# Optimization experiments

Hardware: AMD Instinct MI355X
Metric: run time of the kernel (lower is better)

## Reference

```python
import math
import jax, jax.numpy as jnp
import numpy as np

L, H, C, T_MAX, V = 4, 12, 768, 1024, 50257
D = C // H
EPS = 1e-5


def setup_inputs() -> dict:
    key = jax.random.key(0)
    ks = iter(jax.random.split(key, 32))
    s = 0.02
    inp = {
        "idx": jax.random.randint(next(ks), (2, 1024), 0, V, dtype=jnp.int32),
        "wte": jax.random.normal(next(ks), (V, C), jnp.float32) * s,
        "wpe": jax.random.normal(next(ks), (T_MAX, C), jnp.float32) * s,
        # per-layer stacked params, weights stored [in, out]
        "ln1_w": jnp.ones((L, C), jnp.float32),
        "ln1_b": jnp.zeros((L, C), jnp.float32),
        "qkv_w": jax.random.normal(next(ks), (L, C, 3 * C), jnp.float32) * s,
        "qkv_b": jnp.zeros((L, 3 * C), jnp.float32),
        "proj_w": jax.random.normal(next(ks), (L, C, C), jnp.float32) * (s / math.sqrt(2 * L)),
        "proj_b": jnp.zeros((L, C), jnp.float32),
        "ln2_w": jnp.ones((L, C), jnp.float32),
        "ln2_b": jnp.zeros((L, C), jnp.float32),
        "fc_w": jax.random.normal(next(ks), (L, C, 4 * C), jnp.float32) * s,
        "fc_b": jnp.zeros((L, 4 * C), jnp.float32),
        "fc2_w": jax.random.normal(next(ks), (L, 4 * C, C), jnp.float32) * (s / math.sqrt(2 * L)),
        "fc2_b": jnp.zeros((L, C), jnp.float32),
        "lnf_w": jnp.ones((C,), jnp.float32),
        "lnf_b": jnp.zeros((C,), jnp.float32),
        "head_w": jax.random.normal(next(ks), (C, V), jnp.float32) * s,
    }
    return inp


def _layernorm(x, w, b):
    mu = jnp.mean(x, axis=-1, keepdims=True)
    var = jnp.mean(jnp.square(x - mu), axis=-1, keepdims=True)
    return (x - mu) * jax.lax.rsqrt(var + EPS) * w + b


def _new_gelu(x):
    k = math.sqrt(2.0 / math.pi)
    return 0.5 * x * (1.0 + jnp.tanh(k * (x + 0.044715 * x * x * x)))


def _gpt_forward(idx, wte, wpe, layer_params, lnf_w, lnf_b, head_w):
    B, T = idx.shape
    x = wte[idx] + wpe[:T][None, :, :]  # [B, T, C]
    causal = jnp.tril(jnp.ones((T, T), bool))

    def block(x, p):
        ln1w, ln1b, qkvw, qkvb, pw, pb, ln2w, ln2b, fcw, fcb, fc2w, fc2b = p
        h = _layernorm(x, ln1w, ln1b)
        qkv = h @ qkvw + qkvb  # [B, T, 3C]
        q, k, v = jnp.split(qkv, 3, axis=-1)
        # [B, H, T, D]
        q = q.reshape(B, T, H, D).transpose(0, 2, 1, 3)
        k = k.reshape(B, T, H, D).transpose(0, 2, 1, 3)
        v = v.reshape(B, T, H, D).transpose(0, 2, 1, 3)
        att = jnp.einsum("bhtd,bhsd->bhts", q, k) * (1.0 / math.sqrt(D))
        att = jnp.where(causal, att, -jnp.inf)
        att = jax.nn.softmax(att, axis=-1)
        y = jnp.einsum("bhts,bhsd->bhtd", att, v)
        y = y.transpose(0, 2, 1, 3).reshape(B, T, C)
        x = x + (y @ pw + pb)
        h2 = _layernorm(x, ln2w, ln2b)
        m = _new_gelu(h2 @ fcw + fcb) @ fc2w + fc2b
        return x + m, None

    x, _ = jax.lax.scan(block, x, layer_params)
    x = _layernorm(x, lnf_w, lnf_b)
    logits = x @ head_w  # [B, T, V]
    return logits.reshape(B * T, V)


def reference(idx, wte, wpe, ln1_w, ln1_b, qkv_w, qkv_b, proj_w, proj_b,
              ln2_w, ln2_b, fc_w, fc_b, fc2_w, fc2_b, lnf_w, lnf_b, head_w):
    layer_params = (ln1_w, ln1_b, qkv_w, qkv_b, proj_w, proj_b,
                    ln2_w, ln2_b, fc_w, fc_b, fc2_w, fc2_b)
    return _gpt_forward(idx, wte, wpe, layer_params, lnf_w, lnf_b, head_w)
```

## Files before the change

kernel.cpp:

```cpp
#include <hip/hip_runtime.h>
#include <hip/hip_bf16.h>

typedef __hip_bfloat16 bf16;
typedef __attribute__((ext_vector_type(8))) short bf16x8;
typedef __attribute__((ext_vector_type(4))) float f32x4;
typedef __attribute__((ext_vector_type(4), aligned(4))) float f32x4u;

#define NL 4
#define NH 12
#define C 768
#define T 1024
#define NB 2
#define BTOK 2048
#define V 50257
#define DH 64

__device__ __forceinline__ void gload16(const void* g, void* l) {
  __builtin_amdgcn_global_load_lds(
      (const __attribute__((address_space(1))) void*)g,
      (__attribute__((address_space(3))) void*)l, 16, 0, 0);
}

__device__ __forceinline__ float block_sum(float v, float* red) {
#pragma unroll
  for (int off = 32; off; off >>= 1) v += __shfl_down(v, off);
  int lane = threadIdx.x & 63, wid = threadIdx.x >> 6;
  __syncthreads();
  if (lane == 0) red[wid] = v;
  __syncthreads();
  return red[0] + red[1] + red[2] + red[3];
}

__global__ __launch_bounds__(256) void k_transpose_bf16(const float* __restrict__ W,
    bf16* __restrict__ Wt, int K, int N) {
  __shared__ float tile[64][69];
  long zoff = (long)blockIdx.z * K * N;
  W += zoff;
  Wt += zoff;
  int k0 = blockIdx.x * 64, n0 = blockIdx.y * 64;
  int tid = threadIdx.x;
  int rr = tid >> 4, rc = (tid & 15) * 4;
#pragma unroll
  for (int it = 0; it < 4; it++) {
    int k = it * 16 + rr;
    int gn = n0 + rc;
    const float* src = W + (long)(k0 + k) * N + gn;
    if (gn + 3 < N) {
      f32x4 v = *(const f32x4u*)src;
      tile[k][rc] = v[0]; tile[k][rc + 1] = v[1];
      tile[k][rc + 2] = v[2]; tile[k][rc + 3] = v[3];
    } else {
#pragma unroll
      for (int e = 0; e < 4; e++)
        tile[k][rc + e] = (gn + e < N) ? src[e] : 0.0f;
    }
  }
  __syncthreads();
  int wkc = tid & 7;
#pragma unroll
  for (int it = 0; it < 2; it++) {
    int n = it * 32 + (tid >> 3);
    int gn = n0 + n;
    if (gn < N) {
      union { bf16 h[8]; bf16x8 v; } u;
#pragma unroll
      for (int j = 0; j < 8; j++)
        u.h[j] = __float2bfloat16(tile[wkc * 8 + j][n]);
      *(bf16x8*)&Wt[(long)gn * K + k0 + wkc * 8] = u.v;
    }
  }
}

__global__ __launch_bounds__(256) void k_layernorm(const float* __restrict__ x,
    const float* __restrict__ w, const float* __restrict__ b, bf16* __restrict__ out) {
  __shared__ float red[4];
  long row = blockIdx.x;
  const float* xr = x + row * C;
  int t = threadIdx.x;
  float v0 = xr[t], v1 = xr[t + 256], v2 = xr[t + 512];
  float s = block_sum(v0 + v1 + v2, red);
  float mu = s * (1.0f / C);
  float d0 = v0 - mu, d1 = v1 - mu, d2 = v2 - mu;
  float vs = block_sum(d0 * d0 + d1 * d1 + d2 * d2, red);
  float inv = rsqrtf(vs * (1.0f / C) + 1e-5f);
  bf16* orow = out + row * C;
  orow[t]       = __float2bfloat16(d0 * inv * w[t]       + b[t]);
  orow[t + 256] = __float2bfloat16(d1 * inv * w[t + 256] + b[t + 256]);
  orow[t + 512] = __float2bfloat16(d2 * inv * w[t + 512] + b[t + 512]);
}

__global__ __launch_bounds__(256) void k_embed_ln(const int* __restrict__ idx,
    const float* __restrict__ wte, const float* __restrict__ wpe,
    const float* __restrict__ w, const float* __restrict__ b,
    float* __restrict__ x, bf16* __restrict__ out) {
  __shared__ float red[4];
  long row = blockIdx.x;
  int t = threadIdx.x;
  int tok = idx[row];
  int pos = (int)(row & (T - 1));
  const float* we = wte + (long)tok * C;
  const float* pe = wpe + (long)pos * C;
  float v0 = we[t] + pe[t], v1 = we[t + 256] + pe[t + 256], v2 = we[t + 512] + pe[t + 512];
  float* xr = x + row * C;
  xr[t] = v0; xr[t + 256] = v1; xr[t + 512] = v2;
  float s = block_sum(v0 + v1 + v2, red);
  float mu = s * (1.0f / C);
  float d0 = v0 - mu, d1 = v1 - mu, d2 = v2 - mu;
  float vs = block_sum(d0 * d0 + d1 * d1 + d2 * d2, red);
  float inv = rsqrtf(vs * (1.0f / C) + 1e-5f);
  bf16* orow = out + row * C;
  orow[t]       = __float2bfloat16(d0 * inv * w[t]       + b[t]);
  orow[t + 256] = __float2bfloat16(d1 * inv * w[t + 256] + b[t + 256]);
  orow[t + 512] = __float2bfloat16(d2 * inv * w[t + 512] + b[t + 512]);
}

__global__ __launch_bounds__(256) void k_attn(const bf16* __restrict__ q,
    const bf16* __restrict__ k, const bf16* __restrict__ vt,
    bf16* __restrict__ yb) {
  __shared__ __align__(16) bf16 Pl[4][16][72];
  int pr = blockIdx.x, bh = blockIdx.y;
  int b = bh / NH, h = bh % NH;
  int tid = threadIdx.x, w = tid >> 6, lane = tid & 63;
  int l15 = lane & 15, hi = lane >> 4;
  const bf16* qbase = q + (long)bh * T * DH;
  const bf16* kbase = k + (long)bh * T * DH;
  const bf16* vbase = vt + (long)bh * DH * T;

  int qt = blockIdx.z ? (T / 64 - 1 - pr) : pr;
  int qrow = qt * 64 + w * 16 + l15;
  bf16x8 qf0 = *(const bf16x8*)(qbase + (long)qrow * DH + hi * 8);
  bf16x8 qf1 = *(const bf16x8*)(qbase + (long)qrow * DH + 32 + hi * 8);

  f32x4 accy[4] = {};
  float m_run = -1e30f, l_run = 0.f;

  int nkt = qt + 1;
  for (int kt = 0; kt < nkt; kt++) {
    int kv0 = kt * 64;
    f32x4 accs[4] = {};
#pragma unroll
    for (int kvi = 0; kvi < 4; kvi++) {
      const bf16* kr = kbase + (long)(kv0 + kvi * 16 + l15) * DH + hi * 8;
      bf16x8 kf0 = *(const bf16x8*)kr;
      bf16x8 kf1 = *(const bf16x8*)(kr + 32);
      accs[kvi] = __builtin_amdgcn_mfma_f32_16x16x32_bf16(kf0, qf0, accs[kvi], 0, 0, 0);
      accs[kvi] = __builtin_amdgcn_mfma_f32_16x16x32_bf16(kf1, qf1, accs[kvi], 0, 0, 0);
    }
    bool diag = (kt == qt);
    float p[4][4];
    float tmax = -1e30f;
#pragma unroll
    for (int kvi = 0; kvi < 4; kvi++)
#pragma unroll
      for (int rr = 0; rr < 4; rr++) {
        float s = accs[kvi][rr];
        if (diag && (kvi * 16 + hi * 4 + rr > w * 16 + l15)) s = -1e30f;
        p[kvi][rr] = s;
        tmax = fmaxf(tmax, s);
      }
    tmax = fmaxf(tmax, __shfl_xor(tmax, 16));
    tmax = fmaxf(tmax, __shfl_xor(tmax, 32));
    if (!__all(tmax - m_run <= 8.0f)) {
      float m_new = fmaxf(m_run, tmax);
      float scl = __expf(m_run - m_new);
      l_run *= scl;
#pragma unroll
      for (int rr = 0; rr < 4; rr++) {
        float sy = __shfl(scl, hi * 4 + rr);
#pragma unroll
        for (int j = 0; j < 4; j++) accy[j][rr] *= sy;
      }
      m_run = m_new;
    }
    float psum = 0.f;
#pragma unroll
    for (int kvi = 0; kvi < 4; kvi++)
#pragma unroll
      for (int rr = 0; rr < 4; rr++) {
        float e = __expf(p[kvi][rr] - m_run);
        p[kvi][rr] = e;
        psum += e;
      }
    psum += __shfl_xor(psum, 16);
    psum += __shfl_xor(psum, 32);
    l_run += psum;
#pragma unroll
    for (int kvi = 0; kvi < 4; kvi++) {
      union { bf16 hh[2]; unsigned u; } pk0, pk1;
      pk0.hh[0] = __float2bfloat16(p[kvi][0]);
      pk0.hh[1] = __float2bfloat16(p[kvi][1]);
      pk1.hh[0] = __float2bfloat16(p[kvi][2]);
      pk1.hh[1] = __float2bfloat16(p[kvi][3]);
      *(unsigned*)&Pl[w][l15][kvi * 16 + hi * 4]     = pk0.u;
      *(unsigned*)&Pl[w][l15][kvi * 16 + hi * 4 + 2] = pk1.u;
    }
#pragma unroll
    for (int c = 0; c < 2; c++) {
      bf16x8 pf = *(const bf16x8*)&Pl[w][l15][c * 32 + hi * 8];
#pragma unroll
      for (int j = 0; j < 4; j++) {
        const bf16* vr = vbase + (long)(j * 16 + l15) * T + kv0 + c * 32 + hi * 8;
        bf16x8 vf = *(const bf16x8*)vr;
        accy[j] = __builtin_amdgcn_mfma_f32_16x16x32_bf16(pf, vf, accy[j], 0, 0, 0);
      }
    }
  }
  float inv = 1.0f / l_run;
#pragma unroll
  for (int rr = 0; rr < 4; rr++) {
    float li = __shfl(inv, hi * 4 + rr);
    int qg = qt * 64 + w * 16 + hi * 4 + rr;
#pragma unroll
    for (int j = 0; j < 4; j++)
      yb[((long)(b * T + qg)) * C + h * DH + j * 16 + l15] =
          __float2bfloat16(accy[j][rr] * li);
  }
}

__global__ __launch_bounds__(512, 1) void k_head(const bf16* __restrict__ A,
    const bf16* __restrict__ B, float* __restrict__ Cv) {
  __shared__ __align__(16) char lds[131072];
  int hw = blockIdx.y * 8 + blockIdx.x;
  int L = (hw & 7) * 197 + (hw >> 3);
  int mt = L & 7, nt = L >> 3;
  int m0 = mt * 256, n0 = nt * 256;
  int tid = threadIdx.x, lane = tid & 63, wid = tid >> 6;
  int wm = wid >> 2, wn = wid & 3;
  int l15 = lane & 15, hi = lane >> 4, l7 = lane & 7;
  int sg = (lane & 7) ^ (lane >> 3);
  int srA = wid * 8 + (lane >> 3);
  const bf16* Ab = A + (long)(m0 + srA) * 768 + sg * 8;
  const bf16* Bb = B + (long)(n0 + srA) * 768 + sg * 8;
  auto STAGE = [&](int tile, int h) {
    char* dst = lds + (tile & 1) * 65536 + h * 16384 + wid * 1024;
    const bf16* src = (h < 2 ? Ab : Bb) + (long)((h & 1) * 128) * 768 + tile * 64;
    gload16(src, dst);
    gload16(src + 64 * 768, dst + 8192);
  };
  f32x4 acc[8][4] = {};
  STAGE(0, 0); STAGE(0, 1); STAGE(0, 2); STAGE(0, 3); STAGE(1, 0);
  asm volatile("s_waitcnt vmcnt(2)" ::: "memory");
  __builtin_amdgcn_s_barrier();
  int bro = (wn & 1) * 64;
  int g0 = (hi ^ l7) * 16, g1 = ((4 + hi) ^ l7) * 16;
  for (int t = 0; t < 12; t++) {
    char* ha = lds + (t & 1) * 65536 + wm * 16384;
    char* hb = lds + (t & 1) * 65536 + 32768 + (wn >> 1) * 16384;
    bf16x8 af[4], bv[4];
#pragma unroll
    for (int mf = 0; mf < 4; mf++)
      af[mf] = *(const bf16x8*)(ha + (mf * 16 + l15) * 128 + g0);
#pragma unroll
    for (int nf = 0; nf < 4; nf++)
      bv[nf] = *(const bf16x8*)(hb + (bro + nf * 16 + l15) * 128 + g0);
    if (t + 1 < 12) { STAGE(t + 1, 1); STAGE(t + 1, 2); }
    __builtin_amdgcn_s_barrier();
    __builtin_amdgcn_s_setprio(1);
#pragma unroll
    for (int mf = 0; mf < 4; mf++)
#pragma unroll
      for (int nf = 0; nf < 4; nf++)
        acc[mf][nf] = __builtin_amdgcn_mfma_f32_16x16x32_bf16(af[mf], bv[nf], acc[mf][nf], 0, 0, 0);
    __builtin_amdgcn_s_setprio(0);
    __builtin_amdgcn_s_barrier();
#pragma unroll
    for (int mf = 0; mf < 4; mf++)
      af[mf] = *(const bf16x8*)(ha + ((mf + 4) * 16 + l15) * 128 + g0);
    if (t + 1 < 12) STAGE(t + 1, 3);
    __builtin_amdgcn_s_barrier();
    __builtin_amdgcn_s_setprio(1);
#pragma unroll
    for (int mf = 0; mf < 4; mf++)
#pragma unroll
      for (int nf = 0; nf < 4; nf++)
        acc[mf + 4][nf] = __builtin_amdgcn_mfma_f32_16x16x32_bf16(af[mf], bv[nf], acc[mf + 4][nf], 0, 0, 0);
    __builtin_amdgcn_s_setprio(0);
    __builtin_amdgcn_s_barrier();
#pragma unroll
    for (int mf = 0; mf < 4; mf++)
      af[mf] = *(const bf16x8*)(ha + (mf * 16 + l15) * 128 + g1);
#pragma unroll
    for (int nf = 0; nf < 4; nf++)
      bv[nf] = *(const bf16x8*)(hb + (bro + nf * 16 + l15) * 128 + g1);
    __builtin_amdgcn_s_barrier();
    __builtin_amdgcn_s_setprio(1);
#pragma unroll
    for (int mf = 0; mf < 4; mf++)
#pragma unroll
      for (int nf = 0; nf < 4; nf++)
        acc[mf][nf] = __builtin_amdgcn_mfma_f32_16x16x32_bf16(af[mf], bv[nf], acc[mf][nf], 0, 0, 0);
    __builtin_amdgcn_s_setprio(0);
    __builtin_amdgcn_s_barrier();
#pragma unroll
    for (int mf = 0; mf < 4; mf++)
      af[mf] = *(const bf16x8*)(ha + ((mf + 4) * 16 + l15) * 128 + g1);
    if (t + 2 < 12) STAGE(t + 2, 0);
    __builtin_amdgcn_s_barrier();
    __builtin_amdgcn_s_setprio(1);
#pragma unroll
    for (int mf = 0; mf < 4; mf++)
#pragma unroll
      for (int nf = 0; nf < 4; nf++)
        acc[mf + 4][nf] = __builtin_amdgcn_mfma_f32_16x16x32_bf16(af[mf], bv[nf], acc[mf + 4][nf], 0, 0, 0);
    __builtin_amdgcn_s_setprio(0);
    if (t < 11) {
      if (t + 2 < 12) asm volatile("s_waitcnt vmcnt(2)" ::: "memory");
      else            asm volatile("s_waitcnt vmcnt(0)" ::: "memory");
      __builtin_amdgcn_s_barrier();
    }
  }
  __syncthreads();
  float* Cst = (float*)lds;
#pragma unroll
  for (int rnd = 0; rnd < 4; rnd++) {
#pragma unroll
    for (int mfl = 0; mfl < 2; mfl++) {
      int mf = rnd * 2 + mfl;
#pragma unroll
      for (int nf = 0; nf < 4; nf++)
#pragma unroll
        for (int rr = 0; rr < 4; rr++)
          Cst[(wm * 32 + mfl * 16 + hi * 4 + rr) * 260 + wn * 64 + nf * 16 + l15] =
              acc[mf][nf][rr];
    }
    __syncthreads();
#pragma unroll
    for (int s = 0; s < 8; s++) {
      int gid = tid + s * 512;
      int r = gid >> 6, g = gid & 63;
      int grow = m0 + (r >> 5) * 128 + (rnd * 2 + ((r >> 4) & 1)) * 16 + (r & 15);
      int gcol = n0 + g * 4;
      f32x4 vv = *(const f32x4*)&Cst[r * 260 + g * 4];
      float* dst = Cv + (long)grow * V + gcol;
      if (gcol + 3 < V) {
        *(f32x4u*)dst = vv;
      } else {
#pragma unroll
        for (int e = 0; e < 4; e++)
          if (gcol + e < V) dst[e] = vv[e];
      }
    }
    __syncthreads();
  }
}

#define SBK 64
template <int EPI>
__global__ __launch_bounds__(256) void k_gemm_s(const bf16* __restrict__ A,
    const bf16* __restrict__ B, const float* __restrict__ bias,
    void* __restrict__ Cv, int M, int N, int K, int lda, int ldb, int ldc,
    void* __restrict__ Cv2, void* __restrict__ Cv3) {
  __shared__ __align__(16) bf16 As[2][64][SBK];
  __shared__ __align__(16) bf16 Bs[2][128][SBK];
  int nwg = gridDim.x * gridDim.y;
  int hw = blockIdx.y * gridDim.x + blockIdx.x;
  int logical = (hw & 7) * (nwg >> 3) + (hw >> 3);
  int bx = logical % gridDim.x, by = logical / gridDim.x;
  int m0 = bx * 64, n0 = by * 128;
  int tid = threadIdx.x;
  int lane = tid & 63, w = tid >> 6;
  int l15 = lane & 15, hi = lane >> 4, l7 = lane & 7;
  int srow = lane >> 3;
  int sgr = lane & 7;
  int scol = ((sgr ^ srow) << 3);
  f32x4 acc[4][2] = {};
  const bf16* Ag = A + (long)(m0 + w * 8 + srow) * lda + scol;
  const bf16* Bg = B + (long)(n0 + w * 8 + srow) * ldb + scol;
  int NT = K / SBK;
  auto STAGE = [&](int t) {
    int k0 = t * SBK, b = t & 1;
    gload16(Ag + k0,            &As[b][w * 8][0]);
    gload16(Ag + k0 + 32 * lda, &As[b][w * 8 + 32][0]);
    gload16(Bg + k0,            &Bs[b][w * 8][0]);
    gload16(Bg + k0 + 32 * ldb, &Bs[b][w * 8 + 32][0]);
    gload16(Bg + k0 + 64 * ldb, &Bs[b][w * 8 + 64][0]);
    gload16(Bg + k0 + 96 * ldb, &Bs[b][w * 8 + 96][0]);
  };
  STAGE(0);
  STAGE(1);
  int c0 = (hi ^ l7) << 3, c1 = ((4 + hi) ^ l7) << 3;
  for (int t = 0; t < NT; t++) {
    int b = t & 1;
    if (t + 1 < NT) asm volatile("s_waitcnt vmcnt(6)" ::: "memory");
    else            asm volatile("s_waitcnt vmcnt(0)" ::: "memory");
    __builtin_amdgcn_s_barrier();
    bf16x8 a0[4], a1[4], b0[2], b1[2];
#pragma unroll
    for (int i = 0; i < 4; i++) {
      a0[i] = *(const bf16x8*)&As[b][i * 16 + l15][c0];
      a1[i] = *(const bf16x8*)&As[b][i * 16 + l15][c1];
    }
#pragma unroll
    for (int j = 0; j < 2; j++) {
      b0[j] = *(const bf16x8*)&Bs[b][w * 32 + j * 16 + l15][c0];
      b1[j] = *(const bf16x8*)&Bs[b][w * 32 + j * 16 + l15][c1];
    }
    asm volatile("s_waitcnt lgkmcnt(0)" ::: "memory");
    __builtin_amdgcn_s_barrier();
    if (t + 2 < NT) STAGE(t + 2);
    __builtin_amdgcn_s_setprio(1);
#pragma unroll
    for (int i = 0; i < 4; i++)
#pragma unroll
      for (int j = 0; j < 2; j++) {
        acc[i][j] = __builtin_amdgcn_mfma_f32_16x16x32_bf16(a0[i], b0[j], acc[i][j], 0, 0, 0);
        acc[i][j] = __builtin_amdgcn_mfma_f32_16x16x32_bf16(a1[i], b1[j], acc[i][j], 0, 0, 0);
      }
    __builtin_amdgcn_s_setprio(0);
  }
#pragma unroll
  for (int j = 0; j < 2; j++) {
    int gn = n0 + w * 32 + j * 16 + l15;
    float bv = bias[gn];
#pragma unroll
    for (int i = 0; i < 4; i++)
#pragma unroll
      for (int rr = 0; rr < 4; rr++) {
        int gm = m0 + i * 16 + hi * 4 + rr;
        float v = acc[i][j][rr] + bv;
        if constexpr (EPI == 3) {
          long off = (long)gm * ldc + gn;
          ((float*)Cv)[off] = v + ((float*)Cv)[off];
        } else if constexpr (EPI == 2) {
          float u = 0.7978845608028654f * (v + 0.044715f * v * v * v);
          u = fminf(fmaxf(u, -15.f), 15.f);
          float e2 = __expf(2.f * u);
          float th = (e2 - 1.f) / (e2 + 1.f);
          ((bf16*)Cv)[(long)gm * ldc + gn] = __float2bfloat16(0.5f * v * (1.f + th));
        } else if constexpr (EPI == 5) {
          int gb = gm >> 10, gt = gm & 1023;
          int which = gn / C;
          int r = gn - which * C;
          int h = r >> 6, d = r & 63;
          long bh = (long)(gb * NH + h);
          if (which == 0)
            ((bf16*)Cv)[(bh * T + gt) * DH + d] = __float2bfloat16(v * 0.125f);
          else if (which == 1)
            ((bf16*)Cv2)[(bh * T + gt) * DH + d] = __float2bfloat16(v);
          else
            ((bf16*)Cv3)[(bh * DH + d) * T + gt] = __float2bfloat16(v);
        }
      }
  }
}

extern "C" void kernel_launch(void* const* d_in, const int* in_sizes, int n_in,
                              void* d_out, int out_size, void* d_ws, size_t ws_size,
                              hipStream_t stream) {
  const int*   idx    = (const int*)d_in[0];
  const float* wte    = (const float*)d_in[1];
  const float* wpe    = (const float*)d_in[2];
  const float* ln1_w  = (const float*)d_in[3];
  const float* ln1_b  = (const float*)d_in[4];
  const float* qkv_w  = (const float*)d_in[5];
  const float* qkv_b  = (const float*)d_in[6];
  const float* proj_w = (const float*)d_in[7];
  const float* proj_b = (const float*)d_in[8];
  const float* ln2_w  = (const float*)d_in[9];
  const float* ln2_b  = (const float*)d_in[10];
  const float* fc_w   = (const float*)d_in[11];
  const float* fc_b   = (const float*)d_in[12];
  const float* fc2_w  = (const float*)d_in[13];
  const float* fc2_b  = (const float*)d_in[14];
  const float* lnf_w  = (const float*)d_in[15];
  const float* lnf_b  = (const float*)d_in[16];
  const float* head_w = (const float*)d_in[17];
  (void)in_sizes; (void)n_in; (void)out_size; (void)ws_size;

  char* base = (char*)d_ws;
  size_t off = 0;
  auto alloc = [&](size_t bytes) -> void* {
    void* p = base + off;
    off = (off + bytes + 255) & ~(size_t)255;
    return p;
  };
  bf16* wt_qkv  = (bf16*)alloc((size_t)NL * 3 * C * C * 2);
  bf16* wt_proj = (bf16*)alloc((size_t)NL * C * C * 2);
  bf16* wt_fc   = (bf16*)alloc((size_t)NL * 4 * C * C * 2);
  bf16* wt_fc2  = (bf16*)alloc((size_t)NL * 4 * C * C * 2);
  bf16* wt_head = (bf16*)alloc((size_t)V * C * 2);
  float* x      = (float*)alloc((size_t)BTOK * C * 4);
  bf16*  xb     = (bf16*)alloc((size_t)BTOK * C * 2);
  bf16*  qb     = (bf16*)alloc((size_t)NB * NH * T * DH * 2);
  bf16*  kb     = (bf16*)alloc((size_t)NB * NH * T * DH * 2);
  bf16*  vtb    = (bf16*)alloc((size_t)NB * NH * T * DH * 2);
  bf16*  yb     = (bf16*)alloc((size_t)BTOK * C * 2);
  bf16*  mbuf   = (bf16*)alloc((size_t)BTOK * 4 * C * 2);

  k_transpose_bf16<<<dim3(12, 36, NL), 256, 0, stream>>>(qkv_w, wt_qkv, C, 3 * C);
  k_transpose_bf16<<<dim3(12, 12, NL), 256, 0, stream>>>(proj_w, wt_proj, C, C);
  k_transpose_bf16<<<dim3(12, 48, NL), 256, 0, stream>>>(fc_w, wt_fc, C, 4 * C);
  k_transpose_bf16<<<dim3(48, 12, NL), 256, 0, stream>>>(fc2_w, wt_fc2, 4 * C, C);
  k_transpose_bf16<<<dim3(12, (V + 63) / 64, 1), 256, 0, stream>>>(head_w, wt_head, C, V);

  k_embed_ln<<<BTOK, 256, 0, stream>>>(idx, wte, wpe, ln1_w, ln1_b, x, xb);

  for (int l = 0; l < NL; l++) {
    if (l > 0)
      k_layernorm<<<BTOK, 256, 0, stream>>>(x, ln1_w + l * C, ln1_b + l * C, xb);
    k_gemm_s<5><<<dim3(32, 18), 256, 0, stream>>>(xb, wt_qkv + (long)l * 3 * C * C,
        qkv_b + l * 3 * C, qb, BTOK, 3 * C, C, C, C, 0, kb, vtb);
    k_attn<<<dim3(T / 128, NB * NH, 2), 256, 0, stream>>>(qb, kb, vtb, yb);
    k_gemm_s<3><<<dim3(32, 6), 256, 0, stream>>>(yb, wt_proj + (long)l * C * C,
        proj_b + l * C, x, BTOK, C, C, C, C, C, nullptr, nullptr);
    k_layernorm<<<BTOK, 256, 0, stream>>>(x, ln2_w + l * C, ln2_b + l * C, xb);
    k_gemm_s<2><<<dim3(32, 24), 256, 0, stream>>>(xb, wt_fc + (long)l * 4 * C * C,
        fc_b + l * 4 * C, mbuf, BTOK, 4 * C, C, C, C, 4 * C, nullptr, nullptr);
    k_gemm_s<3><<<dim3(32, 6), 256, 0, stream>>>(mbuf, wt_fc2 + (long)l * 4 * C * C,
        fc2_b + l * C, x, BTOK, C, 4 * C, 4 * C, 4 * C, C, nullptr, nullptr);
  }
  k_layernorm<<<BTOK, 256, 0, stream>>>(x, lnf_w, lnf_b, xb);
  k_head<<<dim3(8, 197), 512, 0, stream>>>(xb, wt_head, (float*)d_out);
}
```

Before: 986.0 us.

## Restructure LM-head GEMM with smaller K tiles and halved LDS for occupancy

Rewrites the vocab-projection GEMM main loop to use 32-wide K tiles (24 iterations) in a simple double-buffered LDS scheme with a new XOR swizzle, halving shared memory from 128KB to 64KB. It also raises the launch-bounds occupancy hint so more blocks can be resident per CU, and splits the epilogue into eight 16-row rounds. The aim is to hide latency through occupancy instead of the previous finely interleaved single-block schedule. The risk is register pressure: 128 accumulator floats under a higher occupancy hint may spill, and shorter K tiles mean more barriers per FLOP.

```diff
diff --git a/kernel.cpp b/kernel.cpp
--- a/kernel.cpp
+++ b/kernel.cpp
@@ -217,118 +217,74 @@
   }
 }
 
-__global__ __launch_bounds__(512, 1) void k_head(const bf16* __restrict__ A,
+__global__ __launch_bounds__(512, 4) void k_head(const bf16* __restrict__ A,
     const bf16* __restrict__ B, float* __restrict__ Cv) {
-  __shared__ __align__(16) char lds[131072];
+  __shared__ __align__(16) char lds[65536];
   int hw = blockIdx.y * 8 + blockIdx.x;
   int L = (hw & 7) * 197 + (hw >> 3);
   int mt = L & 7, nt = L >> 3;
   int m0 = mt * 256, n0 = nt * 256;
   int tid = threadIdx.x, lane = tid & 63, wid = tid >> 6;
   int wm = wid >> 2, wn = wid & 3;
-  int l15 = lane & 15, hi = lane >> 4, l7 = lane & 7;
-  int sg = (lane & 7) ^ (lane >> 3);
-  int srA = wid * 8 + (lane >> 3);
-  const bf16* Ab = A + (long)(m0 + srA) * 768 + sg * 8;
-  const bf16* Bb = B + (long)(n0 + srA) * 768 + sg * 8;
-  auto STAGE = [&](int tile, int h) {
-    char* dst = lds + (tile & 1) * 65536 + h * 16384 + wid * 1024;
-    const bf16* src = (h < 2 ? Ab : Bb) + (long)((h & 1) * 128) * 768 + tile * 64;
-    gload16(src, dst);
-    gload16(src + 64 * 768, dst + 8192);
+  int l15 = lane & 15, hi = lane >> 4;
+  int srow = lane >> 2;
+  int sgsrc = ((lane & 3) ^ ((lane >> 3) & 3)) * 8;
+  const bf16* Ag = A + (long)(m0 + srow) * 768 + sgsrc;
+  const bf16* Bg = B + (long)(n0 + srow) * 768 + sgsrc;
+  const int NT = 24;
+  auto STAGE = [&](int t) {
+    int k0 = t * 32, b = t & 1;
+#pragma unroll
+    for (int q = 0; q < 2; q++) {
+      int R0 = wid * 32 + q * 16;
+      gload16(Ag + (long)R0 * 768 + k0, lds + b * 16384 + R0 * 64);
+      gload16(Bg + (long)R0 * 768 + k0, lds + 32768 + b * 16384 + R0 * 64);
+    }
   };
   f32x4 acc[8][4] = {};
-  STAGE(0, 0); STAGE(0, 1); STAGE(0, 2); STAGE(0, 3); STAGE(1, 0);
-  asm volatile("s_waitcnt vmcnt(2)" ::: "memory");
-  __builtin_amdgcn_s_barrier();
-  int bro = (wn & 1) * 64;
-  int g0 = (hi ^ l7) * 16, g1 = ((4 + hi) ^ l7) * 16;
-  for (int t = 0; t < 12; t++) {
-    char* ha = lds + (t & 1) * 65536 + wm * 16384;
-    char* hb = lds + (t & 1) * 65536 + 32768 + (wn >> 1) * 16384;
-    bf16x8 af[4], bv[4];
-#pragma unroll
-    for (int mf = 0; mf < 4; mf++)
-      af[mf] = *(const bf16x8*)(ha + (mf * 16 + l15) * 128 + g0);
+  STAGE(0);
+  STAGE(1);
+  int gsw = (hi ^ ((l15 >> 1) & 3)) << 4;
+  for (int t = 0; t < NT; t++) {
+    int b = t & 1;
+    if (t + 1 < NT) asm volatile("s_waitcnt vmcnt(4)" ::: "memory");
+    else            asm volatile("s_waitcnt vmcnt(0)" ::: "memory");
+    __builtin_amdgcn_s_barrier();
+    bf16x8 af[8], bv[4];
+    char* ha = lds + b * 16384;
+    char* hb = lds + 32768 + b * 16384;
+#pragma unroll
+    for (int mf = 0; mf < 8; mf++)
+      af[mf] = *(const bf16x8*)(ha + (wm * 128 + mf * 16 + l15) * 64 + gsw);
 #pragma unroll
     for (int nf = 0; nf < 4; nf++)
-      bv[nf] = *(const bf16x8*)(hb + (bro + nf * 16 + l15) * 128 + g0);
-    if (t + 1 < 12) { STAGE(t + 1, 1); STAGE(t + 1, 2); }
+      bv[nf] = *(const bf16x8*)(hb + (wn * 64 + nf * 16 + l15) * 64 + gsw);
+    asm volatile("s_waitcnt lgkmcnt(0)" ::: "memory");
     __builtin_amdgcn_s_barrier();
+    if (t + 2 < NT) STAGE(t + 2);
     __builtin_amdgcn_s_setprio(1);
 #pragma unroll
-    for (int mf = 0; mf < 4; mf++)
+    for (int mf = 0; mf < 8; mf++)
 #pragma unroll
       for (int nf = 0; nf < 4; nf++)
         acc[mf][nf] = __builtin_amdgcn_mfma_f32_16x16x32_bf16(af[mf], bv[nf], acc[mf][nf], 0, 0, 0);
     __builtin_amdgcn_s_setprio(0);
-    __builtin_amdgcn_s_barrier();
-#pragma unroll
-    for (int mf = 0; mf < 4; mf++)
-      af[mf] = *(const bf16x8*)(ha + ((mf + 4) * 16 + l15) * 128 + g0);
-    if (t + 1 < 12) STAGE(t + 1, 3);
-    __builtin_amdgcn_s_barrier();
-    __builtin_amdgcn_s_setprio(1);
-#pragma unroll
-    for (int mf = 0; mf < 4; mf++)
-#pragma unroll
-      for (int nf = 0; nf < 4; nf++)
-        acc[mf + 4][nf] = __builtin_amdgcn_mfma_f32_16x16x32_bf16(af[mf], bv[nf], acc[mf + 4][nf], 0, 0, 0);
-    __builtin_amdgcn_s_setprio(0);
-    __builtin_amdgcn_s_barrier();
-#pragma unroll
-    for (int mf = 0; mf < 4; mf++)
-      af[mf] = *(const bf16x8*)(ha + (mf * 16 + l15) * 128 + g1);
-#pragma unroll
-    for (int nf = 0; nf < 4; nf++)
-      bv[nf] = *(const bf16x8*)(hb + (bro + nf * 16 + l15) * 128 + g1);
-    __builtin_amdgcn_s_barrier();
-    __builtin_amdgcn_s_setprio(1);
-#pragma unroll
-    for (int mf = 0; mf < 4; mf++)
-#pragma unroll
-      for (int nf = 0; nf < 4; nf++)
-        acc[mf][nf] = __builtin_amdgcn_mfma_f32_16x16x32_bf16(af[mf], bv[nf], acc[mf][nf], 0, 0, 0);
-    __builtin_amdgcn_s_setprio(0);
-    __builtin_amdgcn_s_barrier();
-#pragma unroll
-    for (int mf = 0; mf < 4; mf++)
-      af[mf] = *(const bf16x8*)(ha + ((mf + 4) * 16 + l15) * 128 + g1);
-    if (t + 2 < 12) STAGE(t + 2, 0);
-    __builtin_amdgcn_s_barrier();
-    __builtin_amdgcn_s_setprio(1);
-#pragma unroll
-    for (int mf = 0; mf < 4; mf++)
-#pragma unroll
-      for (int nf = 0; nf < 4; nf++)
-        acc[mf + 4][nf] = __builtin_amdgcn_mfma_f32_16x16x32_bf16(af[mf], bv[nf], acc[mf + 4][nf], 0, 0, 0);
-    __builtin_amdgcn_s_setprio(0);
-    if (t < 11) {
-      if (t + 2 < 12) asm volatile("s_waitcnt vmcnt(2)" ::: "memory");
-      else            asm volatile("s_waitcnt vmcnt(0)" ::: "memory");
-      __builtin_amdgcn_s_barrier();
-    }
   }
   __syncthreads();
   float* Cst = (float*)lds;
 #pragma unroll
-  for (int rnd = 0; rnd < 4; rnd++) {
-#pragma unroll
-    for (int mfl = 0; mfl < 2; mfl++) {
-      int mf = rnd * 2 + mfl;
-#pragma unroll
-      for (int nf = 0; nf < 4; nf++)
-#pragma unroll
-        for (int rr = 0; rr < 4; rr++)
-          Cst[(wm * 32 + mfl * 16 + hi * 4 + rr) * 260 + wn * 64 + nf * 16 + l15] =
-              acc[mf][nf][rr];
-    }
+  for (int mf = 0; mf < 8; mf++) {
+#pragma unroll
+    for (int nf = 0; nf < 4; nf++)
+#pragma unroll
+      for (int rr = 0; rr < 4; rr++)
+        Cst[(wm * 16 + hi * 4 + rr) * 260 + wn * 64 + nf * 16 + l15] = acc[mf][nf][rr];
     __syncthreads();
 #pragma unroll
-    for (int s = 0; s < 8; s++) {
+    for (int s = 0; s < 4; s++) {
       int gid = tid + s * 512;
       int r = gid >> 6, g = gid & 63;
-      int grow = m0 + (r >> 5) * 128 + (rnd * 2 + ((r >> 4) & 1)) * 16 + (r & 15);
+      int grow = m0 + (r >> 4) * 128 + mf * 16 + (r & 15);
       int gcol = n0 + g * 4;
       f32x4 vv = *(const f32x4*)&Cst[r * 260 + g * 4];
       float* dst = Cv + (long)grow * V + gcol;
```

After: 2.418 ms. 145% more time.
